# Kernel optimization log

Hardware: AMD Instinct MI355X
Metric: run time of the kernel (lower is better)

The kernel has to match this reference:

```python
import jax, jax.numpy as jnp
import numpy as np

ATTN_BLOCK_SIZE = 1024
NUM_BUCKETS = 32  # int(sqrt(1024))


def _bucket_index():
    # Static index matching the torch init:
    # arange2 = ((arange1 - indices) % S) // num_buckets, then pick columns arange(nb)*nb
    S, nb = ATTN_BLOCK_SIZE, NUM_BUCKETS
    ar = np.arange(S)
    a2 = ((ar[:, None] - ar[None, :]) % S) // nb          # (S, S), values in [0, nb)
    a2 = a2[:, np.arange(nb) * nb]                         # (S, nb)
    return jnp.asarray(a2, dtype=jnp.int32)


def _decay_sum(x, alpha, beta, past_steps):
    # result[t] = alpha * sum_{i=0}^{P-1} beta**i * x[t-1-i]  (zeros for t-1-i < 0)
    # == the torch pad-and-add loop, expressed as one causal depthwise conv.
    B, S, D = x.shape
    P = past_steps
    w = alpha * beta ** jnp.arange(P, dtype=x.dtype)       # (P,) decay weights
    k = jnp.broadcast_to(w[::-1][None, None, :], (D, 1, P))  # depthwise kernel (O=D, I/g=1, W=P)
    xc = jnp.transpose(x, (0, 2, 1))                       # (B, D, S)
    y = jax.lax.conv_general_dilated(
        xc, k, window_strides=(1,), padding=[(P, 0)],
        dimension_numbers=('NCW', 'OIW', 'NCW'), feature_group_count=D,
    )[..., :S]                                             # (B, D, S)
    return jnp.transpose(y, (0, 2, 1))                     # (B, S, D)


def setup_inputs() -> dict:
    key = jax.random.key(0)
    k1, k2, k3, k4, k5 = jax.random.split(key, 5)
    B, S, nb = 1024, ATTN_BLOCK_SIZE, NUM_BUCKETS
    return {
        "x": jax.random.normal(k1, (B, S, nb), dtype=jnp.float32),
        "alpha": jax.random.uniform(k2, (1,), dtype=jnp.float32),
        "beta": jax.random.uniform(k3, (1,), dtype=jnp.float32),
        "pos_fwd_param": jax.random.normal(k4, (1, nb), dtype=jnp.float32),
        "pos_bwd_param": jax.random.normal(k5, (1, nb), dtype=jnp.float32),
        "past_steps": 128,
    }


def reference(x, alpha, beta, pos_fwd_param, pos_bwd_param, past_steps):
    S = ATTN_BLOCK_SIZE
    result = _decay_sum(x, alpha, beta, past_steps)        # (B, S, nb)
    ones = jnp.ones((S, 1), dtype=x.dtype)
    pb_fwd = ones @ pos_fwd_param                          # (S, nb)
    pb_bwd = jnp.take_along_axis(ones @ pos_bwd_param, _bucket_index(), axis=-1)  # (S, nb)
    return result + pb_fwd + pb_bwd
```

## Files before the change

### kernel.cpp

```cpp
#include <hip/hip_runtime.h>


constexpr int S     = 1024;
constexpr int D     = 32;
constexpr int L     = 512;
constexpr int HALO  = 128;
constexpr int TROWS = L + HALO;
constexpr int CHAIN = 64;
constexpr int NTHR  = D * (L / CHAIN);

__global__ __launch_bounds__(NTHR)
void attn_pred_kernel(const float* __restrict__ x,
                      const float* __restrict__ alpha_p,
                      const float* __restrict__ beta_p,
                      const float* __restrict__ pos_fwd,
                      const float* __restrict__ pos_bwd,
                      const int*   __restrict__ past_p,
                      float* __restrict__ out)
{
    __shared__ float xs[TROWS * D];

    const int tid = threadIdx.x;
    const int b   = blockIdx.x >> 1;
    const int s0  = (blockIdx.x & 1) * L;

    const float alpha = alpha_p[0];
    const float beta  = beta_p[0];
    const int   P     = past_p[0];

    double bp = 1.0;
    for (int i = 0; i < P; ++i) bp *= (double)beta;
    const float abP = alpha * (float)bp;

    const float4* xg  = reinterpret_cast<const float4*>(x + (size_t)b * S * D);
    float4*       xs4 = reinterpret_cast<float4*>(xs);
    const int base_row = s0 - HALO;
    #pragma unroll
    for (int k = tid; k < TROWS * (D / 4); k += NTHR) {
        const int r = k >> 3;
        const int s = base_row + r;
        float4 v = make_float4(0.f, 0.f, 0.f, 0.f);
        if (s >= 0) v = xg[(size_t)s * (D / 4) + (k & 7)];
        xs4[k] = v;
    }
    __syncthreads();

    const int d      = tid & (D - 1);
    const int chunk  = tid >> 5;
    const int sstart = s0 + chunk * CHAIN;
    const int rstart = HALO + chunk * CHAIN;

    const float pfv = pos_fwd[d];
    const float pbv = pos_bwd[d];

    float yhat = 0.f;
    const int r0 = rstart - P;
    #pragma unroll 16
    for (int j = 0; j < P; ++j)
        yhat = yhat * beta + xs[(r0 + j) * D + d];
    float y = alpha * yhat;

    float* og = out + ((size_t)b * S + sstart) * D + d;
    #pragma unroll
    for (int h = 0; h < CHAIN / 32; ++h) {
        const int q = (sstart >> 5) + h;
        const float pbc = __shfl(pbv, (q - d) & (D - 1), 64);
        #pragma unroll 8
        for (int i2 = 0; i2 < 32; ++i2) {
            const int i   = h * 32 + i2;
            og[i * D] = y + pfv + pbc;
            const int row = rstart + i;
            const float xt = xs[row * D + d];
            const float xl = xs[(row - P) * D + d];
            y = beta * y + alpha * xt - abP * xl;
        }
    }
}

extern "C" void kernel_launch(void* const* d_in, const int* in_sizes, int n_in,
                              void* d_out, int out_size, void* d_ws, size_t ws_size,
                              hipStream_t stream) {
    const float* x  = (const float*)d_in[0];
    const float* al = (const float*)d_in[1];
    const float* be = (const float*)d_in[2];
    const float* pf = (const float*)d_in[3];
    const float* pb = (const float*)d_in[4];
    const int*   ps = (const int*)d_in[5];
    float* out = (float*)d_out;

    const int B = in_sizes[0] / (S * D);
    dim3 grid(B * (S / L));
    attn_pred_kernel<<<grid, NTHR, 0, stream>>>(x, al, be, pf, pb, ps, out);
}
```

Baseline: 263.3 us.

## Drop shared-memory staging; read x via float4 global loads per thread

Removes the shared-memory tile with its halo and barrier. Each thread now owns four channels (float4) and a 32-step chunk, reads its P-step warm-up window and the lagged values straight from global memory, and writes float4 outputs. One block covers a whole batch row of 256 threads. The aim is to drop the LDS copy, the sync and the duplicated halo. In exchange, the 128-step warm-up is re-read from global or L2 by every chunk, which raises redundant global traffic, and the stride-32 row accesses give poorer coalescing.

```diff
diff --git a/kernel.cpp b/kernel.cpp
--- a/kernel.cpp
+++ b/kernel.cpp
@@ -3,11 +3,8 @@
 
 constexpr int S     = 1024;
 constexpr int D     = 32;
-constexpr int L     = 512;
-constexpr int HALO  = 128;
-constexpr int TROWS = L + HALO;
-constexpr int CHAIN = 64;
-constexpr int NTHR  = D * (L / CHAIN);
+constexpr int CHAIN = 32;
+constexpr int NTHR  = (S / CHAIN) * (D / 4);
 
 __global__ __launch_bounds__(NTHR)
 void attn_pred_kernel(const float* __restrict__ x,
@@ -18,11 +15,11 @@
                       const int*   __restrict__ past_p,
                       float* __restrict__ out)
 {
-    __shared__ float xs[TROWS * D];
-
-    const int tid = threadIdx.x;
-    const int b   = blockIdx.x >> 1;
-    const int s0  = (blockIdx.x & 1) * L;
+    const int tid   = threadIdx.x;
+    const int b     = blockIdx.x;
+    const int dg    = tid & 7;
+    const int chunk = tid >> 3;
+    const int sstart = chunk * CHAIN;
 
     const float alpha = alpha_p[0];
     const float beta  = beta_p[0];
@@ -32,48 +29,47 @@
     for (int i = 0; i < P; ++i) bp *= (double)beta;
     const float abP = alpha * (float)bp;
 
-    const float4* xg  = reinterpret_cast<const float4*>(x + (size_t)b * S * D);
-    float4*       xs4 = reinterpret_cast<float4*>(xs);
-    const int base_row = s0 - HALO;
-    #pragma unroll
-    for (int k = tid; k < TROWS * (D / 4); k += NTHR) {
-        const int r = k >> 3;
-        const int s = base_row + r;
+    const float4* xg = reinterpret_cast<const float4*>(x) + (size_t)b * S * (D / 4);
+
+    float4 y = make_float4(0.f, 0.f, 0.f, 0.f);
+    const int sbase = sstart - P;
+    #pragma unroll 8
+    for (int j = 0; j < P; ++j) {
+        const int s = sbase + j;
         float4 v = make_float4(0.f, 0.f, 0.f, 0.f);
-        if (s >= 0) v = xg[(size_t)s * (D / 4) + (k & 7)];
-        xs4[k] = v;
+        if (s >= 0) v = xg[s * (D / 4) + dg];
+        y.x = fmaf(y.x, beta, v.x);
+        y.y = fmaf(y.y, beta, v.y);
+        y.z = fmaf(y.z, beta, v.z);
+        y.w = fmaf(y.w, beta, v.w);
     }
-    __syncthreads();
+    y.x *= alpha; y.y *= alpha; y.z *= alpha; y.w *= alpha;
 
-    const int d      = tid & (D - 1);
-    const int chunk  = tid >> 5;
-    const int sstart = s0 + chunk * CHAIN;
-    const int rstart = HALO + chunk * CHAIN;
+    const int d0 = dg * 4;
+    const float4 pf = reinterpret_cast<const float4*>(pos_fwd)[dg];
+    float4 add;
+    add.x = pf.x + pos_bwd[(chunk - (d0 + 0)) & (D - 1)];
+    add.y = pf.y + pos_bwd[(chunk - (d0 + 1)) & (D - 1)];
+    add.z = pf.z + pos_bwd[(chunk - (d0 + 2)) & (D - 1)];
+    add.w = pf.w + pos_bwd[(chunk - (d0 + 3)) & (D - 1)];
 
-    const float pfv = pos_fwd[d];
-    const float pbv = pos_bwd[d];
+    float4* og = reinterpret_cast<float4*>(out) + ((size_t)b * S + sstart) * (D / 4) + dg;
+    #pragma unroll 8
+    for (int i = 0; i < CHAIN; ++i) {
+        float4 o;
+        o.x = y.x + add.x; o.y = y.y + add.y; o.z = y.z + add.z; o.w = y.w + add.w;
+        og[i * (D / 4)] = o;
 
-    float yhat = 0.f;
-    const int r0 = rstart - P;
-    #pragma unroll 16
-    for (int j = 0; j < P; ++j)
-        yhat = yhat * beta + xs[(r0 + j) * D + d];
-    float y = alpha * yhat;
+        const int s  = sstart + i;
+        const int sl = s - P;
+        const float4 xt = xg[s * (D / 4) + dg];
+        float4 xl = make_float4(0.f, 0.f, 0.f, 0.f);
+        if (sl >= 0) xl = xg[sl * (D / 4) + dg];
 
-    float* og = out + ((size_t)b * S + sstart) * D + d;
-    #pragma unroll
-    for (int h = 0; h < CHAIN / 32; ++h) {
-        const int q = (sstart >> 5) + h;
-        const float pbc = __shfl(pbv, (q - d) & (D - 1), 64);
-        #pragma unroll 8
-        for (int i2 = 0; i2 < 32; ++i2) {
-            const int i   = h * 32 + i2;
-            og[i * D] = y + pfv + pbc;
-            const int row = rstart + i;
-            const float xt = xs[row * D + d];
-            const float xl = xs[(row - P) * D + d];
-            y = beta * y + alpha * xt - abP * xl;
-        }
+        y.x = fmaf(beta, y.x, fmaf(alpha, xt.x, -abP * xl.x));
+        y.y = fmaf(beta, y.y, fmaf(alpha, xt.y, -abP * xl.y));
+        y.z = fmaf(beta, y.z, fmaf(alpha, xt.z, -abP * xl.z));
+        y.w = fmaf(beta, y.w, fmaf(alpha, xt.w, -abP * xl.w));
     }
 }
 
@@ -89,6 +85,5 @@
     float* out = (float*)d_out;
 
     const int B = in_sizes[0] / (S * D);
-    dim3 grid(B * (S / L));
-    attn_pred_kernel<<<grid, NTHR, 0, stream>>>(x, al, be, pf, pb, ps, out);
+    attn_pred_kernel<<<dim3(B), NTHR, 0, stream>>>(x, al, be, pf, pb, ps, out);
 }
```

Result: slower. 318.7 us (+21.0%).
